# Performance work log

Hardware: AMD Instinct MI355X
Metric: run time of the kernel (lower is better)

## Reference

```python
import jax, jax.numpy as jnp
import numpy as np

B, P, C, D, H = 32, 2048, 19, 512, 4
DH = D // H  # 128
EPS = 1e-5


def setup_inputs() -> dict:
    key = jax.random.key(0)
    ks = jax.random.split(key, 12)
    s = 0.02
    return {
        "x": jax.random.normal(ks[0], (B, P, D), jnp.float32),
        "channel_embeddings": jax.random.normal(ks[1], (C, D), jnp.float32),
        "Wq": jax.random.normal(ks[2], (D, D), jnp.float32) * s,
        "bq": jnp.zeros((D,), jnp.float32),
        "Wk": jax.random.normal(ks[3], (D, D), jnp.float32) * s,
        "bk": jnp.zeros((D,), jnp.float32),
        "Wv": jax.random.normal(ks[4], (D, D), jnp.float32) * s,
        "bv": jnp.zeros((D,), jnp.float32),
        "Wo": jax.random.normal(ks[5], (D, D), jnp.float32) * s,
        "bo": jnp.zeros((D,), jnp.float32),
        "gamma": jnp.ones((D,), jnp.float32),
        "beta": jnp.zeros((D,), jnp.float32),
    }


def reference(x, channel_embeddings, Wq, bq, Wk, bk, Wv, bv, Wo, bo, gamma, beta):
    # q: (B, P, H, DH)
    q = (x @ Wq.T + bq).reshape(B, P, H, DH)
    # K/V depend only on channel embeddings (same for every batch/patch in the
    # original; it merely materialized the broadcast). Compute once: (C, H, DH)
    k = (channel_embeddings @ Wk.T + bk).reshape(C, H, DH)
    v = (channel_embeddings @ Wv.T + bv).reshape(C, H, DH)
    # scores over channels: (B, P, C, H)
    scores = jnp.einsum("bphd,chd->bpch", q, k) / jnp.sqrt(jnp.float32(DH))
    weights = jax.nn.softmax(scores, axis=2)  # softmax over channel dim
    # weighted sum of channel values: (B, P, H, DH) -> (B, P, D)
    attended = jnp.einsum("bpch,chd->bphd", weights, v).reshape(B, P, D)
    out = attended @ Wo.T + bo  # dropout is identity in eval mode
    # residual + layernorm
    h = x + out
    mean = jnp.mean(h, axis=-1, keepdims=True)
    var = jnp.mean(jnp.square(h - mean), axis=-1, keepdims=True)
    return (h - mean) * jax.lax.rsqrt(var + EPS) * gamma + beta
```

## Files before the change

kernel.cpp:

```cpp
#include <hip/hip_runtime.h>
#include <hip/hip_bf16.h>

#define B_  32
#define P_  2048
#define C_  19
#define D_  512
#define H_  4
#define DH_ 128
#define NROW (B_*P_)
#define CHP_ 96

typedef float f32x4 __attribute__((ext_vector_type(4)));
typedef short bf16x8 __attribute__((ext_vector_type(8)));
typedef unsigned short ushort4v __attribute__((ext_vector_type(4)));

__device__ __forceinline__ unsigned short f2bf(float f) {
  union { __hip_bfloat16 h; unsigned short s; } u;
  u.h = __float2bfloat16(f);
  return u.s;
}
__device__ __forceinline__ float bf2f(unsigned short h) {
  return __uint_as_float(((unsigned int)h) << 16);
}

__device__ __forceinline__ bf16x8 ld_cvt8(const float* p) {
  f32x4 v0 = *(const f32x4*)p;
  f32x4 v1 = *(const f32x4*)(p + 4);
  bf16x8 a;
  a[0]=(short)f2bf(v0[0]); a[1]=(short)f2bf(v0[1]);
  a[2]=(short)f2bf(v0[2]); a[3]=(short)f2bf(v0[3]);
  a[4]=(short)f2bf(v1[0]); a[5]=(short)f2bf(v1[1]);
  a[6]=(short)f2bf(v1[2]); a[7]=(short)f2bf(v1[3]);
  return a;
}

__global__ __launch_bounds__(256) void prep1(
    const float* __restrict__ ce,
    const float* __restrict__ Wk, const float* __restrict__ bk,
    const float* __restrict__ Wv, const float* __restrict__ bv,
    float* __restrict__ Kg, float* __restrict__ Vg)
{
  int g = blockIdx.x * 256 + threadIdx.x;
  if (g >= 2*C_*D_) return;
  int which = (g >= C_*D_) ? 1 : 0;
  int idx = which ? (g - C_*D_) : g;
  int c = idx >> 9;
  int n = idx & (D_-1);
  const float* w = (which ? Wv : Wk) + (size_t)n * D_;
  const float* e = ce + (size_t)c * D_;
  float s = 0.f;
  #pragma unroll 8
  for (int d = 0; d < D_; ++d) s = fmaf(e[d], w[d], s);
  s += (which ? bv : bk)[n];
  if (which) Vg[idx] = s; else Kg[idx] = s;
}

__global__ __launch_bounds__(512) void prep2(
    const float* __restrict__ Wq, const float* __restrict__ bq,
    const float* __restrict__ Wo,
    const float* __restrict__ Kg, const float* __restrict__ Vg,
    unsigned short* __restrict__ Mtf, unsigned short* __restrict__ Utf,
    float* __restrict__ s0g)
{
  int p = blockIdx.x;
  int m = threadIdx.x;

  const int mt_off = (p>>4)*8192 + (m>>5)*512 + ((((m>>3)&3)<<4) + (p&15))*8 + (m&7);
  const int ut_off = ((m>>4)*3 + (p>>5))*512 + ((((p>>3)&3)<<4) + (m&15))*8 + (p&7);

  int c = p >> 2, h = p & 3;
  if (c >= C_) {
    if (p < 80) { Mtf[mt_off] = 0; if (m == 0) s0g[p] = 0.f; }
    Utf[ut_off] = 0;
    return;
  }
  const float rs128 = 0.08838834764831843f;
  const float* Kr = Kg + c*D_ + h*DH_;
  const float* Vr = Vg + c*D_ + h*DH_;

  float macc = 0.f;
  #pragma unroll 4
  for (int dh = 0; dh < DH_; ++dh)
    macc = fmaf(Wq[(size_t)(h*DH_+dh)*D_ + m], Kr[dh], macc);
  Mtf[mt_off] = f2bf(macc * rs128);

  float uacc = 0.f;
  const float* wor = Wo + (size_t)m*D_ + h*DH_;
  #pragma unroll 4
  for (int dh = 0; dh < DH_; ++dh)
    uacc = fmaf(wor[dh], Vr[dh], uacc);
  Utf[ut_off] = f2bf(uacc);

  if (m == 0) {
    float sa = 0.f;
    const float* bqr = bq + h*DH_;
    for (int dh = 0; dh < DH_; ++dh) sa = fmaf(bqr[dh], Kr[dh], sa);
    s0g[p] = sa * rs128;
  }
}

__global__ __launch_bounds__(256) void fused64(
    const float* __restrict__ x,
    const unsigned short* __restrict__ Mtf,
    const unsigned short* __restrict__ Utf,
    const float* __restrict__ s0g,
    const float* __restrict__ bo,
    const float* __restrict__ gamma, const float* __restrict__ beta,
    float* __restrict__ out)
{
  __shared__ __attribute__((aligned(16))) unsigned short Xbf[64*512];
  __shared__ __attribute__((aligned(16))) unsigned short WaL[64][104];
  __shared__ float rs_[64][2], rq_[64][2];

  const int t    = threadIdx.x;
  const int wave = t >> 6;
  const int lane = t & 63;
  const int lhi  = lane >> 4;
  const int llo  = lane & 15;
  const int row0 = blockIdx.x * 64;
  const int wrow = wave * 16;

  {
    #pragma unroll
    for (int j = 0; j < 16; ++j) {
      bf16x8 a = ld_cvt8(x + (size_t)(row0 + wrow + j)*D_ + lane*8);
      int byteoff = (wrow + j)*1024 + ((lane*16) ^ ((j & 7) << 4));
      *(bf16x8*)((char*)Xbf + byteoff) = a;
    }
  }
  asm volatile("s_waitcnt lgkmcnt(0)" ::: "memory");
  __builtin_amdgcn_sched_barrier(0);

  {
    const char* xb = (const char*)Xbf + (wrow + llo)*1024;
    const int swz = (llo & 7) << 4;
    f32x4 acc0 = (f32x4){0,0,0,0}, acc1 = acc0, acc2 = acc0, acc3 = acc0, acc4 = acc0;
    #pragma unroll
    for (int ks = 0; ks < 16; ++ks) {
      bf16x8 a = *(const bf16x8*)(xb + ((ks*64 + lhi*16) ^ swz));
      acc0 = __builtin_amdgcn_mfma_f32_16x16x32_bf16(a, *(const bf16x8*)(Mtf + 0*8192 + ks*512 + lane*8), acc0, 0, 0, 0);
      acc1 = __builtin_amdgcn_mfma_f32_16x16x32_bf16(a, *(const bf16x8*)(Mtf + 1*8192 + ks*512 + lane*8), acc1, 0, 0, 0);
      acc2 = __builtin_amdgcn_mfma_f32_16x16x32_bf16(a, *(const bf16x8*)(Mtf + 2*8192 + ks*512 + lane*8), acc2, 0, 0, 0);
      acc3 = __builtin_amdgcn_mfma_f32_16x16x32_bf16(a, *(const bf16x8*)(Mtf + 3*8192 + ks*512 + lane*8), acc3, 0, 0, 0);
      acc4 = __builtin_amdgcn_mfma_f32_16x16x32_bf16(a, *(const bf16x8*)(Mtf + 4*8192 + ks*512 + lane*8), acc4, 0, 0, 0);
    }
    const bool dead = (llo >= 12);
    float s0v0 = s0g[llo], s0v1 = s0g[16+llo], s0v2 = s0g[32+llo],
          s0v3 = s0g[48+llo], s0v4 = s0g[64+llo];
    #pragma unroll
    for (int r = 0; r < 4; ++r) {
      float v0 = acc0[r] + s0v0;
      float v1 = acc1[r] + s0v1;
      float v2 = acc2[r] + s0v2;
      float v3 = acc3[r] + s0v3;
      float v4 = dead ? -1e30f : (acc4[r] + s0v4);
      float mx = fmaxf(fmaxf(fmaxf(v0, v1), fmaxf(v2, v3)), v4);
      mx = fmaxf(mx, __shfl_xor(mx, 4, 64));
      mx = fmaxf(mx, __shfl_xor(mx, 8, 64));
      float e0 = __expf(v0 - mx), e1 = __expf(v1 - mx), e2 = __expf(v2 - mx),
            e3 = __expf(v3 - mx), e4 = dead ? 0.f : __expf(v4 - mx);
      float sm = e0 + e1 + e2 + e3 + e4;
      sm += __shfl_xor(sm, 4, 64);
      sm += __shfl_xor(sm, 8, 64);
      float inv = 1.f / sm;
      int lr = wrow + lhi*4 + r;
      WaL[lr][     llo] = f2bf(e0 * inv);
      WaL[lr][16 + llo] = f2bf(e1 * inv);
      WaL[lr][32 + llo] = f2bf(e2 * inv);
      WaL[lr][48 + llo] = f2bf(e3 * inv);
      WaL[lr][64 + llo] = f2bf(e4 * inv);
    }
    *(ushort4v*)&WaL[wrow + lhi*4 + (llo & 3)][80 + (llo >> 2)*4] = (ushort4v){0,0,0,0};
  }
  __syncthreads();

  const int rg = wave >> 1;
  const int cs = wave & 1;
  #pragma unroll
  for (int ha = 0; ha < 2; ++ha) {
    const int hrow = ha * 32;
    f32x4 oacc[16];
    #pragma unroll
    for (int i = 0; i < 16; ++i) oacc[i] = (f32x4){0.f,0.f,0.f,0.f};
    #pragma unroll
    for (int ks = 0; ks < 3; ++ks) {
      bf16x8 a = *(const bf16x8*)&WaL[hrow + rg*16 + llo][ks*32 + lhi*8];
      #pragma unroll
      for (int tile = 0; tile < 16; ++tile) {
        int ntile = cs*16 + tile;
        bf16x8 b = *(const bf16x8*)(Utf + (size_t)(ntile*3 + ks)*512 + lane*8);
        oacc[tile] = __builtin_amdgcn_mfma_f32_16x16x32_bf16(a, b, oacc[tile], 0, 0, 0);
      }
    }

    float s[4] = {0,0,0,0}, q[4] = {0,0,0,0};
    #pragma unroll
    for (int tile = 0; tile < 16; ++tile) {
      int n = cs*256 + tile*16 + llo;
      float bov = bo[n];
      #pragma unroll
      for (int r = 0; r < 4; ++r) {
        int m = hrow + rg*16 + lhi*4 + r;
        float xres = bf2f(*(const unsigned short*)
            ((const char*)Xbf + m*1024 + ((n*2) ^ ((m & 7) << 4))));
        float val = oacc[tile][r] + bov + xres;
        oacc[tile][r] = val;
        s[r] += val;
        q[r] = fmaf(val, val, q[r]);
      }
    }
    #pragma unroll
    for (int r = 0; r < 4; ++r) {
      #pragma unroll
      for (int off = 1; off < 16; off <<= 1) {
        s[r] += __shfl_xor(s[r], off, 64);
        q[r] += __shfl_xor(q[r], off, 64);
      }
    }
    if (llo == 0) {
      #pragma unroll
      for (int r = 0; r < 4; ++r) {
        rs_[hrow + rg*16 + lhi*4 + r][cs] = s[r];
        rq_[hrow + rg*16 + lhi*4 + r][cs] = q[r];
      }
    }
    __syncthreads();
    float mu_r[4], rstd_r[4];
    #pragma unroll
    for (int r = 0; r < 4; ++r) {
      int m = hrow + rg*16 + lhi*4 + r;
      float sum = rs_[m][0] + rs_[m][1];
      float sq  = rq_[m][0] + rq_[m][1];
      float mu  = sum * (1.f/(float)D_);
      float var = sq * (1.f/(float)D_) - mu*mu;
      mu_r[r]   = mu;
      rstd_r[r] = rsqrtf(var + 1e-5f);
    }
    #pragma unroll
    for (int tile = 0; tile < 16; ++tile) {
      int n = cs*256 + tile*16 + llo;
      float g = gamma[n], bt = beta[n];
      #pragma unroll
      for (int r = 0; r < 4; ++r) {
        int m = hrow + rg*16 + lhi*4 + r;
        out[(size_t)(row0 + m)*D_ + n] = (oacc[tile][r] - mu_r[r]) * rstd_r[r] * g + bt;
      }
    }
  }
}

extern "C" void kernel_launch(void* const* d_in, const int* in_sizes, int n_in,
                              void* d_out, int out_size, void* d_ws, size_t ws_size,
                              hipStream_t stream) {
  const float* x     = (const float*)d_in[0];
  const float* ce    = (const float*)d_in[1];
  const float* Wq    = (const float*)d_in[2];
  const float* bq    = (const float*)d_in[3];
  const float* Wk    = (const float*)d_in[4];
  const float* bk    = (const float*)d_in[5];
  const float* Wv    = (const float*)d_in[6];
  const float* bv    = (const float*)d_in[7];
  const float* Wo    = (const float*)d_in[8];
  const float* bo    = (const float*)d_in[9];
  const float* gamma = (const float*)d_in[10];
  const float* beta  = (const float*)d_in[11];
  float* out = (float*)d_out;

  char* ws = (char*)d_ws;
  float* Kg           = (float*)(ws);
  float* Vg           = (float*)(ws + 40960);
  unsigned short* Mtf = (unsigned short*)(ws + 81920);
  unsigned short* Utf = (unsigned short*)(ws + 163840);
  float* s0g          = (float*)(ws + 262144);

  prep1<<<(2*C_*D_)/256, 256, 0, stream>>>(ce, Wk, bk, Wv, bv, Kg, Vg);
  prep2<<<CHP_, 512, 0, stream>>>(Wq, bq, Wo, Kg, Vg, Mtf, Utf, s0g);
  fused64<<<NROW/64, 256, 0, stream>>>(x, Mtf, Utf, s0g, bo, gamma, beta, out);
}
```

Before: 134.4 us.

## Merge prep kernels and switch main kernel to single-wave 16-row blocks

Result: slower. 140.1 us (+4.2%).

```diff
diff --git a/kernel.cpp b/kernel.cpp
--- a/kernel.cpp
+++ b/kernel.cpp
@@ -1,18 +1,15 @@
 #include <hip/hip_runtime.h>
 #include <hip/hip_bf16.h>
 
-#define B_  32
-#define P_  2048
 #define C_  19
 #define D_  512
 #define H_  4
 #define DH_ 128
-#define NROW (B_*P_)
+#define NROW 65536
 #define CHP_ 96
 
 typedef float f32x4 __attribute__((ext_vector_type(4)));
 typedef short bf16x8 __attribute__((ext_vector_type(8)));
-typedef unsigned short ushort4v __attribute__((ext_vector_type(4)));
 
 __device__ __forceinline__ unsigned short f2bf(float f) {
   union { __hip_bfloat16 h; unsigned short s; } u;
@@ -22,7 +19,6 @@
 __device__ __forceinline__ float bf2f(unsigned short h) {
   return __uint_as_float(((unsigned int)h) << 16);
 }
-
 __device__ __forceinline__ bf16x8 ld_cvt8(const float* p) {
   f32x4 v0 = *(const f32x4*)p;
   f32x4 v1 = *(const f32x4*)(p + 4);
@@ -34,105 +30,96 @@
   return a;
 }
 
-__global__ __launch_bounds__(256) void prep1(
+__global__ __launch_bounds__(512) void prep(
     const float* __restrict__ ce,
+    const float* __restrict__ Wq, const float* __restrict__ bq,
     const float* __restrict__ Wk, const float* __restrict__ bk,
     const float* __restrict__ Wv, const float* __restrict__ bv,
-    float* __restrict__ Kg, float* __restrict__ Vg)
-{
-  int g = blockIdx.x * 256 + threadIdx.x;
-  if (g >= 2*C_*D_) return;
-  int which = (g >= C_*D_) ? 1 : 0;
-  int idx = which ? (g - C_*D_) : g;
-  int c = idx >> 9;
-  int n = idx & (D_-1);
-  const float* w = (which ? Wv : Wk) + (size_t)n * D_;
-  const float* e = ce + (size_t)c * D_;
-  float s = 0.f;
-  #pragma unroll 8
-  for (int d = 0; d < D_; ++d) s = fmaf(e[d], w[d], s);
-  s += (which ? bv : bk)[n];
-  if (which) Vg[idx] = s; else Kg[idx] = s;
-}
-
-__global__ __launch_bounds__(512) void prep2(
-    const float* __restrict__ Wq, const float* __restrict__ bq,
-    const float* __restrict__ Wo,
-    const float* __restrict__ Kg, const float* __restrict__ Vg,
+    const float* __restrict__ Wo, const float* __restrict__ bo,
     unsigned short* __restrict__ Mtf, unsigned short* __restrict__ Utf,
     float* __restrict__ s0g)
 {
-  int p = blockIdx.x;
-  int m = threadIdx.x;
-
+  __shared__ float KV[2][DH_];
+  __shared__ float KVp[512];
+
+  const int p = blockIdx.x;
+  const int m = threadIdx.x;
   const int mt_off = (p>>4)*8192 + (m>>5)*512 + ((((m>>3)&3)<<4) + (p&15))*8 + (m&7);
   const int ut_off = ((m>>4)*3 + (p>>5))*512 + ((((p>>3)&3)<<4) + (m&15))*8 + (p&7);
-
-  int c = p >> 2, h = p & 3;
+  const int c = p >> 2, h = p & 3;
+
   if (c >= C_) {
     if (p < 80) { Mtf[mt_off] = 0; if (m == 0) s0g[p] = 0.f; }
-    Utf[ut_off] = 0;
+    Utf[ut_off] = (p == 80) ? f2bf(bo[m]) : (unsigned short)0;
     return;
   }
+
+  {
+    const int which = m >> 8;
+    const int dh    = (m >> 1) & 127;
+    const int half  = m & 1;
+    const float* w = (which ? Wv : Wk) + (size_t)(h*DH_ + dh)*D_ + half*256;
+    const float* e = ce + (size_t)c*D_ + half*256;
+    float acc = 0.f;
+    #pragma unroll 8
+    for (int d = 0; d < 256; ++d) acc = fmaf(e[d], w[d], acc);
+    KVp[m] = acc;
+  }
+  __syncthreads();
+  if (m < 256) {
+    const int which = m >> 7, dh = m & 127;
+    KV[which][dh] = KVp[2*m] + KVp[2*m+1] + (which ? bv : bk)[h*DH_ + dh];
+  }
+  __syncthreads();
+
   const float rs128 = 0.08838834764831843f;
-  const float* Kr = Kg + c*D_ + h*DH_;
-  const float* Vr = Vg + c*D_ + h*DH_;
-
   float macc = 0.f;
   #pragma unroll 4
   for (int dh = 0; dh < DH_; ++dh)
-    macc = fmaf(Wq[(size_t)(h*DH_+dh)*D_ + m], Kr[dh], macc);
+    macc = fmaf(Wq[(size_t)(h*DH_+dh)*D_ + m], KV[0][dh], macc);
   Mtf[mt_off] = f2bf(macc * rs128);
 
   float uacc = 0.f;
   const float* wor = Wo + (size_t)m*D_ + h*DH_;
   #pragma unroll 4
   for (int dh = 0; dh < DH_; ++dh)
-    uacc = fmaf(wor[dh], Vr[dh], uacc);
+    uacc = fmaf(wor[dh], KV[1][dh], uacc);
   Utf[ut_off] = f2bf(uacc);
 
   if (m == 0) {
     float sa = 0.f;
-    const float* bqr = bq + h*DH_;
-    for (int dh = 0; dh < DH_; ++dh) sa = fmaf(bqr[dh], Kr[dh], sa);
+    for (int dh = 0; dh < DH_; ++dh) sa = fmaf(bq[h*DH_+dh], KV[0][dh], sa);
     s0g[p] = sa * rs128;
   }
 }
 
-__global__ __launch_bounds__(256) void fused64(
+__global__ __launch_bounds__(64, 2) void fused16w(
     const float* __restrict__ x,
     const unsigned short* __restrict__ Mtf,
     const unsigned short* __restrict__ Utf,
     const float* __restrict__ s0g,
-    const float* __restrict__ bo,
     const float* __restrict__ gamma, const float* __restrict__ beta,
     float* __restrict__ out)
 {
-  __shared__ __attribute__((aligned(16))) unsigned short Xbf[64*512];
-  __shared__ __attribute__((aligned(16))) unsigned short WaL[64][104];
-  __shared__ float rs_[64][2], rq_[64][2];
-
-  const int t    = threadIdx.x;
-  const int wave = t >> 6;
-  const int lane = t & 63;
+  __shared__ __attribute__((aligned(16))) unsigned short Xbf[16*512];
+  __shared__ __attribute__((aligned(16))) unsigned short WaL[16][104];
+
+  const int lane = threadIdx.x;
   const int lhi  = lane >> 4;
   const int llo  = lane & 15;
-  const int row0 = blockIdx.x * 64;
-  const int wrow = wave * 16;
-
-  {
-    #pragma unroll
-    for (int j = 0; j < 16; ++j) {
-      bf16x8 a = ld_cvt8(x + (size_t)(row0 + wrow + j)*D_ + lane*8);
-      int byteoff = (wrow + j)*1024 + ((lane*16) ^ ((j & 7) << 4));
-      *(bf16x8*)((char*)Xbf + byteoff) = a;
-    }
+  const int row0 = blockIdx.x * 16;
+
+  #pragma unroll
+  for (int j = 0; j < 16; ++j) {
+    bf16x8 a = ld_cvt8(x + (size_t)(row0 + j)*D_ + lane*8);
+    int byteoff = j*1024 + ((lane*16) ^ ((j & 7) << 4));
+    *(bf16x8*)((char*)Xbf + byteoff) = a;
   }
   asm volatile("s_waitcnt lgkmcnt(0)" ::: "memory");
   __builtin_amdgcn_sched_barrier(0);
 
   {
-    const char* xb = (const char*)Xbf + (wrow + llo)*1024;
+    const char* xb = (const char*)Xbf + llo*1024;
     const int swz = (llo & 7) << 4;
     f32x4 acc0 = (f32x4){0,0,0,0}, acc1 = acc0, acc2 = acc0, acc3 = acc0, acc4 = acc0;
     #pragma unroll
@@ -163,88 +150,77 @@
       sm += __shfl_xor(sm, 4, 64);
       sm += __shfl_xor(sm, 8, 64);
       float inv = 1.f / sm;
-      int lr = wrow + lhi*4 + r;
+      int lr = lhi*4 + r;
       WaL[lr][     llo] = f2bf(e0 * inv);
       WaL[lr][16 + llo] = f2bf(e1 * inv);
       WaL[lr][32 + llo] = f2bf(e2 * inv);
       WaL[lr][48 + llo] = f2bf(e3 * inv);
       WaL[lr][64 + llo] = f2bf(e4 * inv);
     }
-    *(ushort4v*)&WaL[wrow + lhi*4 + (llo & 3)][80 + (llo >> 2)*4] = (ushort4v){0,0,0,0};
-  }
-  __syncthreads();
-
-  const int rg = wave >> 1;
-  const int cs = wave & 1;
-  #pragma unroll
-  for (int ha = 0; ha < 2; ++ha) {
-    const int hrow = ha * 32;
-    f32x4 oacc[16];
-    #pragma unroll
-    for (int i = 0; i < 16; ++i) oacc[i] = (f32x4){0.f,0.f,0.f,0.f};
-    #pragma unroll
-    for (int ks = 0; ks < 3; ++ks) {
-      bf16x8 a = *(const bf16x8*)&WaL[hrow + rg*16 + llo][ks*32 + lhi*8];
-      #pragma unroll
-      for (int tile = 0; tile < 16; ++tile) {
-        int ntile = cs*16 + tile;
-        bf16x8 b = *(const bf16x8*)(Utf + (size_t)(ntile*3 + ks)*512 + lane*8);
-        oacc[tile] = __builtin_amdgcn_mfma_f32_16x16x32_bf16(a, b, oacc[tile], 0, 0, 0);
-      }
-    }
-
-    float s[4] = {0,0,0,0}, q[4] = {0,0,0,0};
-    #pragma unroll
-    for (int tile = 0; tile < 16; ++tile) {
-      int n = cs*256 + tile*16 + llo;
-      float bov = bo[n];
-      #pragma unroll
-      for (int r = 0; r < 4; ++r) {
-        int m = hrow + rg*16 + lhi*4 + r;
-        float xres = bf2f(*(const unsigned short*)
-            ((const char*)Xbf + m*1024 + ((n*2) ^ ((m & 7) << 4))));
-        float val = oacc[tile][r] + bov + xres;
-        oacc[tile][r] = val;
-        s[r] += val;
-        q[r] = fmaf(val, val, q[r]);
-      }
-    }
+    {
+      int prow = lhi*4 + (llo & 3);
+      int cj   = llo >> 2;
+      unsigned short v0 = (cj == 0) ? (unsigned short)0x3F80 : (unsigned short)0;
+      WaL[prow][80 + cj*4 + 0] = v0;
+      WaL[prow][80 + cj*4 + 1] = 0;
+      WaL[prow][80 + cj*4 + 2] = 0;
+      WaL[prow][80 + cj*4 + 3] = 0;
+    }
+  }
+  asm volatile("s_waitcnt lgkmcnt(0)" ::: "memory");
+  __builtin_amdgcn_sched_barrier(0);
+
+  f32x4 oacc[32];
+  #pragma unroll
+  for (int i = 0; i < 32; ++i) oacc[i] = (f32x4){0.f,0.f,0.f,0.f};
+  #pragma unroll
+  for (int ks = 0; ks < 3; ++ks) {
+    bf16x8 a = *(const bf16x8*)&WaL[llo][ks*32 + lhi*8];
+    #pragma unroll
+    for (int t = 0; t < 32; ++t) {
+      bf16x8 b = *(const bf16x8*)(Utf + (size_t)(t*3 + ks)*512 + lane*8);
+      oacc[t] = __builtin_amdgcn_mfma_f32_16x16x32_bf16(a, b, oacc[t], 0, 0, 0);
+    }
+  }
+
+  float s[4] = {0,0,0,0}, q[4] = {0,0,0,0};
+  #pragma unroll
+  for (int t = 0; t < 32; ++t) {
+    int n = t*16 + llo;
     #pragma unroll
     for (int r = 0; r < 4; ++r) {
-      #pragma unroll
-      for (int off = 1; off < 16; off <<= 1) {
-        s[r] += __shfl_xor(s[r], off, 64);
-        q[r] += __shfl_xor(q[r], off, 64);
-      }
-    }
-    if (llo == 0) {
-      #pragma unroll
-      for (int r = 0; r < 4; ++r) {
-        rs_[hrow + rg*16 + lhi*4 + r][cs] = s[r];
-        rq_[hrow + rg*16 + lhi*4 + r][cs] = q[r];
-      }
-    }
-    __syncthreads();
-    float mu_r[4], rstd_r[4];
+      int mr = lhi*4 + r;
+      float xres = bf2f(*(const unsigned short*)
+          ((const char*)Xbf + mr*1024 + ((n*2) ^ ((mr & 7) << 4))));
+      float val = oacc[t][r] + xres;
+      oacc[t][r] = val;
+      s[r] += val;
+      q[r] = fmaf(val, val, q[r]);
+    }
+  }
+  #pragma unroll
+  for (int r = 0; r < 4; ++r) {
+    #pragma unroll
+    for (int off = 1; off < 16; off <<= 1) {
+      s[r] += __shfl_xor(s[r], off, 64);
+      q[r] += __shfl_xor(q[r], off, 64);
+    }
+  }
+  float mu_r[4], rstd_r[4];
+  #pragma unroll
+  for (int r = 0; r < 4; ++r) {
+    float mu  = s[r] * (1.f/(float)D_);
+    float var = q[r] * (1.f/(float)D_) - mu*mu;
+    mu_r[r]   = mu;
+    rstd_r[r] = rsqrtf(var + 1e-5f);
+  }
+  #pragma unroll
+  for (int t = 0; t < 32; ++t) {
+    int n = t*16 + llo;
+    float g = gamma[n], bt = beta[n];
     #pragma unroll
     for (int r = 0; r < 4; ++r) {
-      int m = hrow + rg*16 + lhi*4 + r;
-      float sum = rs_[m][0] + rs_[m][1];
-      float sq  = rq_[m][0] + rq_[m][1];
-      float mu  = sum * (1.f/(float)D_);
-      float var = sq * (1.f/(float)D_) - mu*mu;
-      mu_r[r]   = mu;
-      rstd_r[r] = rsqrtf(var + 1e-5f);
-    }
-    #pragma unroll
-    for (int tile = 0; tile < 16; ++tile) {
-      int n = cs*256 + tile*16 + llo;
-      float g = gamma[n], bt = beta[n];
-      #pragma unroll
-      for (int r = 0; r < 4; ++r) {
-        int m = hrow + rg*16 + lhi*4 + r;
-        out[(size_t)(row0 + m)*D_ + n] = (oacc[tile][r] - mu_r[r]) * rstd_r[r] * g + bt;
-      }
+      out[(size_t)(row0 + lhi*4 + r)*D_ + n] = (oacc[t][r] - mu_r[r]) * rstd_r[r] * g + bt;
     }
   }
 }
@@ -267,13 +243,11 @@
   float* out = (float*)d_out;
 
   char* ws = (char*)d_ws;
-  float* Kg           = (float*)(ws);
-  float* Vg           = (float*)(ws + 40960);
-  unsigned short* Mtf = (unsigned short*)(ws + 81920);
-  unsigned short* Utf = (unsigned short*)(ws + 163840);
-  float* s0g          = (float*)(ws + 262144);
-
-  prep1<<<(2*C_*D_)/256, 256, 0, stream>>>(ce, Wk, bk, Wv, bv, Kg, Vg);
-  prep2<<<CHP_, 512, 0, stream>>>(Wq, bq, Wo, Kg, Vg, Mtf, Utf, s0g);
-  fused64<<<NROW/64, 256, 0, stream>>>(x, Mtf, Utf, s0g, bo, gamma, beta, out);
-}
+  unsigned short* Mtf = (unsigned short*)(ws);
+  unsigned short* Utf = (unsigned short*)(ws + 81920);
+  float* s0g          = (float*)(ws + 180224);
+
+  prep<<<CHP_, 512, 0, stream>>>(ce, Wq, bq, Wk, bk, Wv, bv, Wo, bo,
+                                 Mtf, Utf, s0g);
+  fused16w<<<NROW/16, 64, 0, stream>>>(x, Mtf, Utf, s0g, gamma, beta, out);
+}
```

## Merge prep kernels and fold output bias into padded MFMA column

Applied to the files above, without the earlier changes.

After: 131.7 us, median of 2. 2.0% less time.

```diff
diff --git a/kernel.cpp b/kernel.cpp
--- a/kernel.cpp
+++ b/kernel.cpp
@@ -1,18 +1,15 @@
 #include <hip/hip_runtime.h>
 #include <hip/hip_bf16.h>
 
-#define B_  32
-#define P_  2048
 #define C_  19
 #define D_  512
 #define H_  4
 #define DH_ 128
-#define NROW (B_*P_)
+#define NROW 65536
 #define CHP_ 96
 
 typedef float f32x4 __attribute__((ext_vector_type(4)));
 typedef short bf16x8 __attribute__((ext_vector_type(8)));
-typedef unsigned short ushort4v __attribute__((ext_vector_type(4)));
 
 __device__ __forceinline__ unsigned short f2bf(float f) {
   union { __hip_bfloat16 h; unsigned short s; } u;
@@ -22,7 +19,6 @@
 __device__ __forceinline__ float bf2f(unsigned short h) {
   return __uint_as_float(((unsigned int)h) << 16);
 }
-
 __device__ __forceinline__ bf16x8 ld_cvt8(const float* p) {
   f32x4 v0 = *(const f32x4*)p;
   f32x4 v1 = *(const f32x4*)(p + 4);
@@ -34,67 +30,65 @@
   return a;
 }
 
-__global__ __launch_bounds__(256) void prep1(
+__global__ __launch_bounds__(512) void prep(
     const float* __restrict__ ce,
+    const float* __restrict__ Wq, const float* __restrict__ bq,
     const float* __restrict__ Wk, const float* __restrict__ bk,
     const float* __restrict__ Wv, const float* __restrict__ bv,
-    float* __restrict__ Kg, float* __restrict__ Vg)
-{
-  int g = blockIdx.x * 256 + threadIdx.x;
-  if (g >= 2*C_*D_) return;
-  int which = (g >= C_*D_) ? 1 : 0;
-  int idx = which ? (g - C_*D_) : g;
-  int c = idx >> 9;
-  int n = idx & (D_-1);
-  const float* w = (which ? Wv : Wk) + (size_t)n * D_;
-  const float* e = ce + (size_t)c * D_;
-  float s = 0.f;
-  #pragma unroll 8
-  for (int d = 0; d < D_; ++d) s = fmaf(e[d], w[d], s);
-  s += (which ? bv : bk)[n];
-  if (which) Vg[idx] = s; else Kg[idx] = s;
-}
-
-__global__ __launch_bounds__(512) void prep2(
-    const float* __restrict__ Wq, const float* __restrict__ bq,
-    const float* __restrict__ Wo,
-    const float* __restrict__ Kg, const float* __restrict__ Vg,
+    const float* __restrict__ Wo, const float* __restrict__ bo,
     unsigned short* __restrict__ Mtf, unsigned short* __restrict__ Utf,
     float* __restrict__ s0g)
 {
-  int p = blockIdx.x;
-  int m = threadIdx.x;
-
+  __shared__ float KV[2][DH_];
+  __shared__ float KVp[512];
+
+  const int p = blockIdx.x;
+  const int m = threadIdx.x;
   const int mt_off = (p>>4)*8192 + (m>>5)*512 + ((((m>>3)&3)<<4) + (p&15))*8 + (m&7);
   const int ut_off = ((m>>4)*3 + (p>>5))*512 + ((((p>>3)&3)<<4) + (m&15))*8 + (p&7);
-
-  int c = p >> 2, h = p & 3;
+  const int c = p >> 2, h = p & 3;
+
   if (c >= C_) {
     if (p < 80) { Mtf[mt_off] = 0; if (m == 0) s0g[p] = 0.f; }
-    Utf[ut_off] = 0;
+    Utf[ut_off] = (p == 80) ? f2bf(bo[m]) : (unsigned short)0;
     return;
   }
+
+  {
+    const int which = m >> 8;
+    const int dh    = (m >> 1) & 127;
+    const int half  = m & 1;
+    const float* w = (which ? Wv : Wk) + (size_t)(h*DH_ + dh)*D_ + half*256;
+    const float* e = ce + (size_t)c*D_ + half*256;
+    float acc = 0.f;
+    #pragma unroll 8
+    for (int d = 0; d < 256; ++d) acc = fmaf(e[d], w[d], acc);
+    KVp[m] = acc;
+  }
+  __syncthreads();
+  if (m < 256) {
+    const int which = m >> 7, dh = m & 127;
+    KV[which][dh] = KVp[2*m] + KVp[2*m+1] + (which ? bv : bk)[h*DH_ + dh];
+  }
+  __syncthreads();
+
   const float rs128 = 0.08838834764831843f;
-  const float* Kr = Kg + c*D_ + h*DH_;
-  const float* Vr = Vg + c*D_ + h*DH_;
-
   float macc = 0.f;
   #pragma unroll 4
   for (int dh = 0; dh < DH_; ++dh)
-    macc = fmaf(Wq[(size_t)(h*DH_+dh)*D_ + m], Kr[dh], macc);
+    macc = fmaf(Wq[(size_t)(h*DH_+dh)*D_ + m], KV[0][dh], macc);
   Mtf[mt_off] = f2bf(macc * rs128);
 
   float uacc = 0.f;
   const float* wor = Wo + (size_t)m*D_ + h*DH_;
   #pragma unroll 4
   for (int dh = 0; dh < DH_; ++dh)
-    uacc = fmaf(wor[dh], Vr[dh], uacc);
+    uacc = fmaf(wor[dh], KV[1][dh], uacc);
   Utf[ut_off] = f2bf(uacc);
 
   if (m == 0) {
     float sa = 0.f;
-    const float* bqr = bq + h*DH_;
-    for (int dh = 0; dh < DH_; ++dh) sa = fmaf(bqr[dh], Kr[dh], sa);
+    for (int dh = 0; dh < DH_; ++dh) sa = fmaf(bq[h*DH_+dh], KV[0][dh], sa);
     s0g[p] = sa * rs128;
   }
 }
@@ -104,7 +98,6 @@
     const unsigned short* __restrict__ Mtf,
     const unsigned short* __restrict__ Utf,
     const float* __restrict__ s0g,
-    const float* __restrict__ bo,
     const float* __restrict__ gamma, const float* __restrict__ beta,
     float* __restrict__ out)
 {
@@ -170,7 +163,14 @@
       WaL[lr][48 + llo] = f2bf(e3 * inv);
       WaL[lr][64 + llo] = f2bf(e4 * inv);
     }
-    *(ushort4v*)&WaL[wrow + lhi*4 + (llo & 3)][80 + (llo >> 2)*4] = (ushort4v){0,0,0,0};
+    {
+      int prow = wrow + lhi*4 + (llo & 3);
+      int cj   = llo >> 2;
+      WaL[prow][80 + cj*4 + 0] = (cj == 0) ? (unsigned short)0x3F80 : (unsigned short)0;
+      WaL[prow][80 + cj*4 + 1] = 0;
+      WaL[prow][80 + cj*4 + 2] = 0;
+      WaL[prow][80 + cj*4 + 3] = 0;
+    }
   }
   __syncthreads();
 
@@ -197,13 +197,12 @@
     #pragma unroll
     for (int tile = 0; tile < 16; ++tile) {
       int n = cs*256 + tile*16 + llo;
-      float bov = bo[n];
       #pragma unroll
       for (int r = 0; r < 4; ++r) {
         int m = hrow + rg*16 + lhi*4 + r;
         float xres = bf2f(*(const unsigned short*)
             ((const char*)Xbf + m*1024 + ((n*2) ^ ((m & 7) << 4))));
-        float val = oacc[tile][r] + bov + xres;
+        float val = oacc[tile][r] + xres;
         oacc[tile][r] = val;
         s[r] += val;
         q[r] = fmaf(val, val, q[r]);
@@ -267,13 +266,11 @@
   float* out = (float*)d_out;
 
   char* ws = (char*)d_ws;
-  float* Kg           = (float*)(ws);
-  float* Vg           = (float*)(ws + 40960);
-  unsigned short* Mtf = (unsigned short*)(ws + 81920);
-  unsigned short* Utf = (unsigned short*)(ws + 163840);
-  float* s0g          = (float*)(ws + 262144);
-
-  prep1<<<(2*C_*D_)/256, 256, 0, stream>>>(ce, Wk, bk, Wv, bv, Kg, Vg);
-  prep2<<<CHP_, 512, 0, stream>>>(Wq, bq, Wo, Kg, Vg, Mtf, Utf, s0g);
-  fused64<<<NROW/64, 256, 0, stream>>>(x, Mtf, Utf, s0g, bo, gamma, beta, out);
-}
+  unsigned short* Mtf = (unsigned short*)(ws);
+  unsigned short* Utf = (unsigned short*)(ws + 81920);
+  float* s0g          = (float*)(ws + 180224);
+
+  prep<<<CHP_, 512, 0, stream>>>(ce, Wq, bq, Wk, bk, Wv, bv, Wo, bo,
+                                 Mtf, Utf, s0g);
+  fused64<<<NROW/64, 256, 0, stream>>>(x, Mtf, Utf, s0g, gamma, beta, out);
+}
```
